# Optimization experiments

Measured on AMD Instinct MI355X. Metric: run time of the kernel, lower is better.

The kernel has to match this reference:

```python
import jax, jax.numpy as jnp
import numpy as np

N = 50000   # nodes
E = 800000  # edges
D = 256     # num_features == embedding_num
L = 3       # gcn layers
G = 512     # graphs in batch


def setup_inputs() -> dict:
    key = jax.random.key(0)
    ks = jax.random.split(key, 7)
    x = jax.random.normal(ks[0], (N, D), dtype=jnp.float32)
    edge_index = jax.random.randint(ks[1], (2, E), 0, N, dtype=jnp.int32)
    batch = jnp.sort(jax.random.randint(ks[2], (N,), 0, G, dtype=jnp.int32))
    s = 0.05
    Ws1 = jax.random.normal(ks[3], (L, D, D), dtype=jnp.float32) * s
    bs1 = jnp.zeros((L, D), dtype=jnp.float32)
    Ws2 = jax.random.normal(ks[4], (L, D, D), dtype=jnp.float32) * s
    bs2 = jnp.zeros((L, D), dtype=jnp.float32)
    return {"x": x, "edge_index": edge_index, "batch": batch,
            "Ws1": Ws1, "bs1": bs1, "Ws2": Ws2, "bs2": bs2}


def reference(x, edge_index, batch, Ws1, bs1, Ws2, bs2):
    src, dst = edge_index[0], edge_index[1]
    h = x
    xs = []
    for i in range(L):
        # GINConv (eps=0): h_i' = MLP( h_i + sum_{j->i} h_j )
        agg = h + jax.ops.segment_sum(h[src], dst, num_segments=N)  # [N, D]
        t = jnp.maximum(agg @ Ws1[i] + bs1[i], 0.0)                 # inner ReLU
        h = jnp.maximum(t @ Ws2[i] + bs2[i], 0.0)                   # outer F.relu
        xs.append(h)
    # global mean pool per layer output, keyed by graph id
    ones = jnp.ones((N, 1), dtype=x.dtype)
    counts = jnp.clip(jax.ops.segment_sum(ones, batch, num_segments=G), 1.0)  # [G,1]
    pooled = [jax.ops.segment_sum(h_i, batch, num_segments=G) / counts for h_i in xs]
    graph_embed = jnp.concatenate(pooled, axis=1)  # [G, L*D]
    node_embed = jnp.concatenate(xs, axis=1)       # [N, L*D]
    return graph_embed, node_embed
```

## Files before the change

### kernel.cpp

```cpp
#include <hip/hip_runtime.h>

#define NN 50000
#define EE 800000
#define DD 256
#define LL 3
#define GG 512
#define MPAD 50048

typedef __attribute__((ext_vector_type(4))) _Float16 half4;
typedef __attribute__((ext_vector_type(8))) _Float16 half8;
typedef __attribute__((ext_vector_type(16))) float floatx16;

#define CONV_B 12500
#define WPK_B  192
#define HIST_B 3125

__global__ void k_prep(const float* __restrict__ x, _Float16* __restrict__ h16,
                       const float* __restrict__ Ws1, const float* __restrict__ Ws2,
                       _Float16* __restrict__ Wp,
                       const int* __restrict__ dst, int* __restrict__ deg) {
    int b = blockIdx.x;
    if (b < CONV_B) {
        int i = b * 256 + threadIdx.x;
        if (i >= NN * DD / 4) return;
        float4 v = ((const float4*)x)[i];
        half4 o;
        o.x = (_Float16)v.x; o.y = (_Float16)v.y; o.z = (_Float16)v.z; o.w = (_Float16)v.w;
        ((half4*)h16)[i] = o;
    } else if (b < CONV_B + WPK_B) {
        int tid  = (b - CONV_B) * 256 + threadIdx.x;
        int lane = tid & 63;
        int nb   = (tid >> 6) & 7;
        int ks   = (tid >> 9) & 15;
        int w    = tid >> 13;
        if (w >= 6) return;
        int l = w >> 1, s = w & 1;
        const float* W = (s == 0 ? Ws1 : Ws2) + (size_t)l * DD * DD;
        int kbase = ks * 16 + (lane >> 5) * 8;
        int n     = nb * 32 + (lane & 31);
        half8 hi;
#pragma unroll
        for (int j = 0; j < 8; ++j) hi[j] = (_Float16)W[(size_t)(kbase + j) * DD + n];
        ((half8*)Wp)[(((size_t)w * 16 + ks) * 8 + nb) * 64 + lane] = hi;
    } else {
        int i = (b - CONV_B - WPK_B) * 256 + threadIdx.x;
        if (i < EE) atomicAdd(&deg[dst[i]], 1);
    }
}

__global__ void k_scan1(const int* __restrict__ deg, int* __restrict__ rp,
                        int* __restrict__ bsum, int n) {
    __shared__ int s[1024];
    int t = threadIdx.x;
    int i = blockIdx.x * 1024 + t;
    int v = (i < n) ? deg[i] : 0;
    s[t] = v;
    __syncthreads();
    for (int off = 1; off < 1024; off <<= 1) {
        int tmp = (t >= off) ? s[t - off] : 0;
        __syncthreads();
        s[t] += tmp;
        __syncthreads();
    }
    if (i < n) rp[i] = s[t] - v;
    if (t == 1023) bsum[blockIdx.x] = s[1023];
}

__global__ void k_scan2(int* __restrict__ bsum, int nb, int* __restrict__ total_out) {
    int lane = threadIdx.x & 63;
    int v = (lane < nb) ? bsum[lane] : 0;
    int orig = v;
    for (int off = 1; off < 64; off <<= 1) {
        int u = __shfl_up(v, off);
        if (lane >= off) v += u;
    }
    if (lane < nb) bsum[lane] = v - orig;
    if (lane == 63) *total_out = v;
}

__global__ void k_scan3(int* __restrict__ rp, const int* __restrict__ bsum,
                        int* __restrict__ cursor, int n) {
    int i = blockIdx.x * 1024 + threadIdx.x;
    if (i < n) {
        int v = rp[i] + bsum[blockIdx.x];
        rp[i] = v;
        cursor[i] = v;
    }
}

__global__ void k_scatter(const int* __restrict__ src, const int* __restrict__ dst,
                          int* __restrict__ cursor, int* __restrict__ csr_src, int e) {
    int i = blockIdx.x * blockDim.x + threadIdx.x;
    if (i < e) {
        int d = dst[i];
        int pos = atomicAdd(&cursor[d], 1);
        csr_src[pos] = src[i];
    }
}

__global__ __launch_bounds__(256) void k_gather(
        const _Float16* __restrict__ h,
        const int* __restrict__ row_ptr,
        const int* __restrict__ csr_src,
        _Float16* __restrict__ agg) {
    __shared__ int eidx[1024];
    __shared__ int rp_s[5];
    int t = threadIdx.x, lane = t & 63, w = t >> 6;
    int n0 = blockIdx.x * 4;
    if (t < 5) {
        int nn = n0 + t;
        if (nn > NN) nn = NN;
        rp_s[t] = row_ptr[nn];
    }
    __syncthreads();
    int beg0 = rp_s[0];
    int cnt  = rp_s[4] - beg0;
    for (int i = t; i < cnt && i < 1024; i += 256) eidx[i] = csr_src[beg0 + i];
    __syncthreads();

    int n = n0 + w;
    if (n >= NN) return;
    int beg = rp_s[w] - beg0, end = rp_s[w + 1] - beg0;
    int hf = lane >> 5;
    int cl = lane & 31;
    const half8* hp = (const half8*)h;

    half8 acc;
#pragma unroll
    for (int i = 0; i < 8; ++i) acc[i] = (_Float16)0;
    if (hf == 0) acc = hp[(size_t)n * 32 + cl];

    if (cnt <= 1024) {
        int k = beg;
        for (; k + 16 <= end; k += 16) {
            half8 v[8];
#pragma unroll
            for (int u = 0; u < 8; ++u) {
                int s = eidx[k + 2 * u + hf];
                v[u] = hp[(size_t)s * 32 + cl];
            }
#pragma unroll
            for (int u = 0; u < 8; ++u) acc += v[u];
        }
        if (k < end) {
#pragma unroll
            for (int u = 0; u < 8; ++u) {
                int e = k + 2 * u + hf;
                half8 v;
#pragma unroll
                for (int i = 0; i < 8; ++i) v[i] = (_Float16)0;
                if (e < end) v = hp[(size_t)eidx[e] * 32 + cl];
                acc += v;
            }
        }
    } else {
        int k = beg;
        for (; k + 16 <= end; k += 16) {
            half8 v[8];
#pragma unroll
            for (int u = 0; u < 8; ++u) {
                int s = csr_src[beg0 + k + 2 * u + hf];
                v[u] = hp[(size_t)s * 32 + cl];
            }
#pragma unroll
            for (int u = 0; u < 8; ++u) acc += v[u];
        }
        if (k < end) {
#pragma unroll
            for (int u = 0; u < 8; ++u) {
                int e = k + 2 * u + hf;
                half8 v;
#pragma unroll
                for (int i = 0; i < 8; ++i) v[i] = (_Float16)0;
                if (e < end) v = hp[(size_t)csr_src[beg0 + e] * 32 + cl];
                acc += v;
            }
        }
    }

    int4 ai = *(int4*)&acc;
    int4 bi;
    bi.x = __shfl_xor(ai.x, 32);
    bi.y = __shfl_xor(ai.y, 32);
    bi.z = __shfl_xor(ai.z, 32);
    bi.w = __shfl_xor(ai.w, 32);
    acc += *(half8*)&bi;
    if (hf == 0) ((half8*)(agg + (size_t)n * DD))[cl] = acc;
}

__global__ __launch_bounds__(256) void k_mlp(
        const _Float16* __restrict__ A,
        const int* __restrict__ batch,
        const _Float16* __restrict__ Wp1, const float* __restrict__ b1,
        const _Float16* __restrict__ Wp2, const float* __restrict__ b2,
        _Float16* __restrict__ Hout,
        float* __restrict__ Fout,
        float* __restrict__ Gout) {
    __shared__ _Float16 t_lds[32 * 256];
    __shared__ int batch_s[32];
    int t    = threadIdx.x;
    int lane = t & 63;
    int w    = t >> 6;
    int r0   = blockIdx.x * 32;

    if (t < 32) {
        int r = r0 + t;
        batch_s[t] = (r < NN) ? batch[r] : 0x7fffffff;
    }

    int arow = r0 + (lane & 31);
    const half8* baseA = (const half8*)(A + (size_t)arow * DD) + (lane >> 5);
    const half8* B1    = (const half8*)Wp1;

    floatx16 acc[2];
#pragma unroll
    for (int nt = 0; nt < 2; ++nt)
#pragma unroll
        for (int i = 0; i < 16; ++i) acc[nt][i] = 0.0f;

#pragma unroll 4
    for (int ks = 0; ks < 16; ++ks) {
        half8 a = baseA[ks * 2];
#pragma unroll
        for (int nt = 0; nt < 2; ++nt) {
            half8 b = B1[(size_t)(ks * 8 + w * 2 + nt) * 64 + lane];
            acc[nt] = __builtin_amdgcn_mfma_f32_32x32x16_f16(a, b, acc[nt], 0, 0, 0);
        }
    }

#pragma unroll
    for (int nt = 0; nt < 2; ++nt) {
        int c  = w * 64 + nt * 32 + (lane & 31);
        float bv = b1[c];
#pragma unroll
        for (int reg = 0; reg < 16; ++reg) {
            int lr = (reg & 3) + 8 * (reg >> 2) + 4 * (lane >> 5);
            float v = fmaxf(acc[nt][reg] + bv, 0.0f);
            t_lds[lr * 256 + ((((c >> 3) ^ (lr & 7)) << 3) | (c & 7))] = (_Float16)v;
        }
    }
    __syncthreads();

    const half8* B2 = (const half8*)Wp2;
    int r = lane & 31;
    floatx16 acc2[2];
#pragma unroll
    for (int nt = 0; nt < 2; ++nt)
#pragma unroll
        for (int i = 0; i < 16; ++i) acc2[nt][i] = 0.0f;

#pragma unroll 4
    for (int ks = 0; ks < 16; ++ks) {
        int kblk = ks * 2 + (lane >> 5);
        half8 a = *(const half8*)&t_lds[r * 256 + ((kblk ^ (r & 7)) << 3)];
#pragma unroll
        for (int nt = 0; nt < 2; ++nt) {
            half8 b = B2[(size_t)(ks * 8 + w * 2 + nt) * 64 + lane];
            acc2[nt] = __builtin_amdgcn_mfma_f32_32x32x16_f16(a, b, acc2[nt], 0, 0, 0);
        }
    }

    const int rbase = 4 * (lane >> 5);
#pragma unroll
    for (int nt = 0; nt < 2; ++nt) {
        int col = w * 64 + nt * 32 + (lane & 31);
        float bv = b2[col];
#pragma unroll
        for (int reg = 0; reg < 16; ++reg) {
            int rowid = rbase + (reg & 3) + 8 * (reg >> 2);
            int row = r0 + rowid;
            if (row < NN) {
                float v = fmaxf(acc2[nt][reg] + bv, 0.0f);
                if (Hout) Hout[(size_t)row * DD + col] = (_Float16)v;
                __builtin_nontemporal_store(v, &Fout[(size_t)row * 768 + col]);
            }
        }
    }

    int lastid = NN - 1 - r0;
    if (lastid >= 0) {
        if (lastid > 31) lastid = 31;
        int g0 = batch_s[0];
        int g1 = batch_s[lastid];
        for (int g = g0; g <= g1; ++g) {
#pragma unroll
            for (int nt = 0; nt < 2; ++nt) {
                int col = w * 64 + nt * 32 + (lane & 31);
                float bv = b2[col];
                float s = 0.0f;
#pragma unroll
                for (int reg = 0; reg < 16; ++reg) {
                    int rowid = rbase + (reg & 3) + 8 * (reg >> 2);
                    if (batch_s[rowid] == g)
                        s += fmaxf(acc2[nt][reg] + bv, 0.0f);
                }
                s += __shfl_xor(s, 32);
                if (lane < 32)
                    atomicAdd(&Gout[(size_t)g * 768 + col], s);
            }
        }
    }
}

__global__ void k_pool_final(const float* __restrict__ gsum,
                             const int* __restrict__ batch,
                             float* __restrict__ graph_embed) {
    int g = blockIdx.x;
    int t = threadIdx.x;
    int start, end;
    { int l = 0, h = NN; while (l < h) { int m = (l + h) >> 1; if (batch[m] < g) l = m + 1; else h = m; } start = l; }
    { int l = 0, h = NN; while (l < h) { int m = (l + h) >> 1; if (batch[m] < g + 1) l = m + 1; else h = m; } end = l; }
    int cnt = end - start;
    float inv = 1.0f / (float)(cnt > 0 ? cnt : 1);
    float4 v = ((const float4*)(gsum + (size_t)g * 768))[t];
    float4 o; o.x = v.x * inv; o.y = v.y * inv; o.z = v.z * inv; o.w = v.w * inv;
    ((float4*)(graph_embed + (size_t)g * 768))[t] = o;
}

extern "C" void kernel_launch(void* const* d_in, const int* in_sizes, int n_in,
                              void* d_out, int out_size, void* d_ws, size_t ws_size,
                              hipStream_t stream) {
    const float* x     = (const float*)d_in[0];
    const int*   ei    = (const int*)d_in[1];
    const int*   batch = (const int*)d_in[2];
    const float* Ws1   = (const float*)d_in[3];
    const float* bs1   = (const float*)d_in[4];
    const float* Ws2   = (const float*)d_in[5];
    const float* bs2   = (const float*)d_in[6];

    float* out         = (float*)d_out;
    float* graph_embed = out;
    float* node_embed  = out + (size_t)GG * 768;

    _Float16* h16   = (_Float16*)d_ws;
    _Float16* agg16 = h16 + (size_t)MPAD * DD;
    _Float16* Wp    = agg16 + (size_t)MPAD * DD;
    float* gsum     = (float*)(Wp + (size_t)6 * 65536);
    int* cursor     = (int*)(gsum + (size_t)GG * 768);
    int* bsum       = cursor + NN;
    int* csr_src    = bsum + 64;
    int* row_ptr    = csr_src + EE;

    const int* src = ei;
    const int* dst = ei + EE;

    const int NB = (NN + 1023) / 1024;

    hipMemsetAsync(gsum, 0, (size_t)GG * 768 * 4 + (size_t)NN * 4 + 64 * 4, stream);

    k_prep<<<CONV_B + WPK_B + HIST_B, 256, 0, stream>>>(x, h16, Ws1, Ws2, Wp, dst, cursor);

    k_scan1<<<NB, 1024, 0, stream>>>(cursor, row_ptr, bsum, NN);
    k_scan2<<<1, 64, 0, stream>>>(bsum, NB, row_ptr + NN);
    k_scan3<<<NB, 1024, 0, stream>>>(row_ptr, bsum, cursor, NN);
    k_scatter<<<(EE + 255) / 256, 256, 0, stream>>>(src, dst, cursor, csr_src, EE);

    for (int l = 0; l < LL; ++l) {
        k_gather<<<(NN + 3) / 4, 256, 0, stream>>>(h16, row_ptr, csr_src, agg16);
        k_mlp<<<MPAD / 32, 256, 0, stream>>>(
            agg16, batch,
            Wp + (size_t)(2 * l + 0) * 65536, bs1 + (size_t)l * DD,
            Wp + (size_t)(2 * l + 1) * 65536, bs2 + (size_t)l * DD,
            (l == LL - 1) ? nullptr : h16,
            node_embed + (size_t)l * DD, gsum + (size_t)l * DD);
    }

    k_pool_final<<<GG, 192, 0, stream>>>(gsum, batch, graph_embed);
}
```

Measured before the change: 594.8 us.

## Pipeline gather and MLP across node chunks in a combined kernel

Splits each layer's node range into four chunks and launches a combined kernel whose blocks either run the MLP on the previous chunk or gather the next chunk. The goal is to overlap the memory-bound gather with the compute-bound MLP instead of running them as separate full-size launches. The hidden state is now double-buffered (h16/h_alt) so the next layer's output is not written while another chunk still reads the current layer's input. This adds launches per layer and uses more shared memory per block in the combined kernel, which may lower occupancy.

```diff
diff --git a/kernel.cpp b/kernel.cpp
--- a/kernel.cpp
+++ b/kernel.cpp
@@ -6,6 +6,9 @@
 #define LL 3
 #define GG 512
 #define MPAD 50048
+#define RPC  12512
+#define GB   (RPC / 4)
+#define MB   (RPC / 32)
 
 typedef __attribute__((ext_vector_type(4))) _Float16 half4;
 typedef __attribute__((ext_vector_type(8))) _Float16 half8;
@@ -98,15 +101,12 @@
     }
 }
 
-__global__ __launch_bounds__(256) void k_gather(
+__device__ __forceinline__ void gather_body(
         const _Float16* __restrict__ h,
         const int* __restrict__ row_ptr,
         const int* __restrict__ csr_src,
-        _Float16* __restrict__ agg) {
-    __shared__ int eidx[1024];
-    __shared__ int rp_s[5];
+        _Float16* agg, int n0, int* eidx, int* rp_s) {
     int t = threadIdx.x, lane = t & 63, w = t >> 6;
-    int n0 = blockIdx.x * 4;
     if (t < 5) {
         int nn = n0 + t;
         if (nn > NN) nn = NN;
@@ -188,20 +188,16 @@
     if (hf == 0) ((half8*)(agg + (size_t)n * DD))[cl] = acc;
 }
 
-__global__ __launch_bounds__(256) void k_mlp(
+__device__ __forceinline__ void mlp_body(
         const _Float16* __restrict__ A,
         const int* __restrict__ batch,
         const _Float16* __restrict__ Wp1, const float* __restrict__ b1,
         const _Float16* __restrict__ Wp2, const float* __restrict__ b2,
-        _Float16* __restrict__ Hout,
-        float* __restrict__ Fout,
-        float* __restrict__ Gout) {
-    __shared__ _Float16 t_lds[32 * 256];
-    __shared__ int batch_s[32];
+        _Float16* Hout, float* __restrict__ Fout, float* __restrict__ Gout,
+        int r0, _Float16* t_lds, int* batch_s) {
     int t    = threadIdx.x;
     int lane = t & 63;
     int w    = t >> 6;
-    int r0   = blockIdx.x * 32;
 
     if (t < 32) {
         int r = r0 + t;
@@ -299,6 +295,47 @@
                     atomicAdd(&Gout[(size_t)g * 768 + col], s);
             }
         }
+    }
+}
+
+__global__ __launch_bounds__(256) void k_gather(
+        const _Float16* __restrict__ h, const int* __restrict__ row_ptr,
+        const int* __restrict__ csr_src, _Float16* agg, int nbeg) {
+    __shared__ int eidx[1024];
+    __shared__ int rp_s[5];
+    gather_body(h, row_ptr, csr_src, agg, nbeg + blockIdx.x * 4, eidx, rp_s);
+}
+
+__global__ __launch_bounds__(256) void k_mlp(
+        const _Float16* __restrict__ A, const int* __restrict__ batch,
+        const _Float16* __restrict__ Wp1, const float* __restrict__ b1,
+        const _Float16* __restrict__ Wp2, const float* __restrict__ b2,
+        _Float16* Hout, float* __restrict__ Fout, float* __restrict__ Gout,
+        int rbeg) {
+    __shared__ _Float16 t_lds[32 * 256];
+    __shared__ int batch_s[32];
+    mlp_body(A, batch, Wp1, b1, Wp2, b2, Hout, Fout, Gout,
+             rbeg + blockIdx.x * 32, t_lds, batch_s);
+}
+
+__global__ __launch_bounds__(256) void k_gm(
+        const _Float16* __restrict__ hin, const int* __restrict__ row_ptr,
+        const int* __restrict__ csr_src, _Float16* agg,
+        const int* __restrict__ batch,
+        const _Float16* __restrict__ Wp1, const float* __restrict__ b1,
+        const _Float16* __restrict__ Wp2, const float* __restrict__ b2,
+        _Float16* Hout, float* __restrict__ Fout, float* __restrict__ Gout,
+        int mlp_blocks, int mlp_rbeg, int gather_nbeg) {
+    __shared__ _Float16 t_lds[32 * 256];
+    __shared__ int batch_s[32];
+    __shared__ int eidx[1024];
+    __shared__ int rp_s[5];
+    if ((int)blockIdx.x < mlp_blocks) {
+        mlp_body(agg, batch, Wp1, b1, Wp2, b2, Hout, Fout, Gout,
+                 mlp_rbeg + blockIdx.x * 32, t_lds, batch_s);
+    } else {
+        gather_body(hin, row_ptr, csr_src, agg,
+                    gather_nbeg + (blockIdx.x - mlp_blocks) * 4, eidx, rp_s);
     }
 }
 
@@ -333,7 +370,8 @@
     float* node_embed  = out + (size_t)GG * 768;
 
     _Float16* h16   = (_Float16*)d_ws;
-    _Float16* agg16 = h16 + (size_t)MPAD * DD;
+    _Float16* h_alt = h16 + (size_t)MPAD * DD;
+    _Float16* agg16 = h_alt + (size_t)MPAD * DD;
     _Float16* Wp    = agg16 + (size_t)MPAD * DD;
     float* gsum     = (float*)(Wp + (size_t)6 * 65536);
     int* cursor     = (int*)(gsum + (size_t)GG * 768);
@@ -356,13 +394,23 @@
     k_scatter<<<(EE + 255) / 256, 256, 0, stream>>>(src, dst, cursor, csr_src, EE);
 
     for (int l = 0; l < LL; ++l) {
-        k_gather<<<(NN + 3) / 4, 256, 0, stream>>>(h16, row_ptr, csr_src, agg16);
-        k_mlp<<<MPAD / 32, 256, 0, stream>>>(
-            agg16, batch,
-            Wp + (size_t)(2 * l + 0) * 65536, bs1 + (size_t)l * DD,
-            Wp + (size_t)(2 * l + 1) * 65536, bs2 + (size_t)l * DD,
-            (l == LL - 1) ? nullptr : h16,
-            node_embed + (size_t)l * DD, gsum + (size_t)l * DD);
+        const _Float16* hin  = (l & 1) ? h_alt : h16;
+        _Float16*       hout = (l == LL - 1) ? nullptr : ((l & 1) ? h16 : h_alt);
+        const _Float16* W1 = Wp + (size_t)(2 * l + 0) * 65536;
+        const _Float16* W2 = Wp + (size_t)(2 * l + 1) * 65536;
+        const float* bb1 = bs1 + (size_t)l * DD;
+        const float* bb2 = bs2 + (size_t)l * DD;
+        float* F  = node_embed + (size_t)l * DD;
+        float* Gp = gsum + (size_t)l * DD;
+
+        k_gather<<<GB, 256, 0, stream>>>(hin, row_ptr, csr_src, agg16, 0);
+        for (int c = 0; c < 3; ++c)
+            k_gm<<<MB + GB, 256, 0, stream>>>(
+                hin, row_ptr, csr_src, agg16, batch,
+                W1, bb1, W2, bb2, hout, F, Gp,
+                MB, c * RPC, (c + 1) * RPC);
+        k_mlp<<<MB, 256, 0, stream>>>(agg16, batch, W1, bb1, W2, bb2,
+                                      hout, F, Gp, 3 * RPC);
     }
 
     k_pool_final<<<GG, 192, 0, stream>>>(gsum, batch, graph_embed);
```

New measurement: 607.7 us. +2.2%, slower.

## Fuse neighbor gather into MLP kernel with ping-pong feature buffers

Applied to the files above, without the earlier changes.

The separate gather and MLP kernels are merged into one per-layer kernel. Each 32-row block now aggregates its own node neighborhoods straight into LDS and feeds that tile to the first MFMA GEMM. This removes the agg16 round trip through global memory and one launch per layer. Because blocks now read h while others write it, the layer input and output alternate between two buffers. In exchange, each block has only 4 waves serially gathering 8 nodes each, which may reduce memory-level parallelism compared with the former 12500-block gather.

```diff
diff --git a/kernel.cpp b/kernel.cpp
--- a/kernel.cpp
+++ b/kernel.cpp
@@ -6,6 +6,7 @@
 #define LL 3
 #define GG 512
 #define MPAD 50048
+#define FB   1563
 
 typedef __attribute__((ext_vector_type(4))) _Float16 half4;
 typedef __attribute__((ext_vector_type(8))) _Float16 half8;
@@ -98,98 +99,10 @@
     }
 }
 
-__global__ __launch_bounds__(256) void k_gather(
-        const _Float16* __restrict__ h,
+__global__ __launch_bounds__(256) void k_layer(
+        const _Float16* __restrict__ hin,
         const int* __restrict__ row_ptr,
         const int* __restrict__ csr_src,
-        _Float16* __restrict__ agg) {
-    __shared__ int eidx[1024];
-    __shared__ int rp_s[5];
-    int t = threadIdx.x, lane = t & 63, w = t >> 6;
-    int n0 = blockIdx.x * 4;
-    if (t < 5) {
-        int nn = n0 + t;
-        if (nn > NN) nn = NN;
-        rp_s[t] = row_ptr[nn];
-    }
-    __syncthreads();
-    int beg0 = rp_s[0];
-    int cnt  = rp_s[4] - beg0;
-    for (int i = t; i < cnt && i < 1024; i += 256) eidx[i] = csr_src[beg0 + i];
-    __syncthreads();
-
-    int n = n0 + w;
-    if (n >= NN) return;
-    int beg = rp_s[w] - beg0, end = rp_s[w + 1] - beg0;
-    int hf = lane >> 5;
-    int cl = lane & 31;
-    const half8* hp = (const half8*)h;
-
-    half8 acc;
-#pragma unroll
-    for (int i = 0; i < 8; ++i) acc[i] = (_Float16)0;
-    if (hf == 0) acc = hp[(size_t)n * 32 + cl];
-
-    if (cnt <= 1024) {
-        int k = beg;
-        for (; k + 16 <= end; k += 16) {
-            half8 v[8];
-#pragma unroll
-            for (int u = 0; u < 8; ++u) {
-                int s = eidx[k + 2 * u + hf];
-                v[u] = hp[(size_t)s * 32 + cl];
-            }
-#pragma unroll
-            for (int u = 0; u < 8; ++u) acc += v[u];
-        }
-        if (k < end) {
-#pragma unroll
-            for (int u = 0; u < 8; ++u) {
-                int e = k + 2 * u + hf;
-                half8 v;
-#pragma unroll
-                for (int i = 0; i < 8; ++i) v[i] = (_Float16)0;
-                if (e < end) v = hp[(size_t)eidx[e] * 32 + cl];
-                acc += v;
-            }
-        }
-    } else {
-        int k = beg;
-        for (; k + 16 <= end; k += 16) {
-            half8 v[8];
-#pragma unroll
-            for (int u = 0; u < 8; ++u) {
-                int s = csr_src[beg0 + k + 2 * u + hf];
-                v[u] = hp[(size_t)s * 32 + cl];
-            }
-#pragma unroll
-            for (int u = 0; u < 8; ++u) acc += v[u];
-        }
-        if (k < end) {
-#pragma unroll
-            for (int u = 0; u < 8; ++u) {
-                int e = k + 2 * u + hf;
-                half8 v;
-#pragma unroll
-                for (int i = 0; i < 8; ++i) v[i] = (_Float16)0;
-                if (e < end) v = hp[(size_t)csr_src[beg0 + e] * 32 + cl];
-                acc += v;
-            }
-        }
-    }
-
-    int4 ai = *(int4*)&acc;
-    int4 bi;
-    bi.x = __shfl_xor(ai.x, 32);
-    bi.y = __shfl_xor(ai.y, 32);
-    bi.z = __shfl_xor(ai.z, 32);
-    bi.w = __shfl_xor(ai.w, 32);
-    acc += *(half8*)&bi;
-    if (hf == 0) ((half8*)(agg + (size_t)n * DD))[cl] = acc;
-}
-
-__global__ __launch_bounds__(256) void k_mlp(
-        const _Float16* __restrict__ A,
         const int* __restrict__ batch,
         const _Float16* __restrict__ Wp1, const float* __restrict__ b1,
         const _Float16* __restrict__ Wp2, const float* __restrict__ b2,
@@ -197,36 +110,123 @@
         float* __restrict__ Fout,
         float* __restrict__ Gout) {
     __shared__ _Float16 t_lds[32 * 256];
+    __shared__ int eidx[1536];
+    __shared__ int rp_s[33];
     __shared__ int batch_s[32];
     int t    = threadIdx.x;
     int lane = t & 63;
     int w    = t >> 6;
     int r0   = blockIdx.x * 32;
 
-    if (t < 32) {
-        int r = r0 + t;
-        batch_s[t] = (r < NN) ? batch[r] : 0x7fffffff;
-    }
-
-    int arow = r0 + (lane & 31);
-    const half8* baseA = (const half8*)(A + (size_t)arow * DD) + (lane >> 5);
-    const half8* B1    = (const half8*)Wp1;
-
-    floatx16 acc[2];
+    if (t < 33) {
+        int nn = r0 + t;
+        if (nn > NN) nn = NN;
+        rp_s[t] = row_ptr[nn];
+    }
+    if (t >= 64 && t < 96) {
+        int r = r0 + (t - 64);
+        batch_s[t - 64] = (r < NN) ? batch[r] : 0x7fffffff;
+    }
+    __syncthreads();
+    int beg0 = rp_s[0];
+    int cnt  = rp_s[32] - beg0;
+    for (int i = t; i < cnt && i < 1536; i += 256) eidx[i] = csr_src[beg0 + i];
+    __syncthreads();
+
+    int hf = lane >> 5;
+    int cl = lane & 31;
+    const half8* hp = (const half8*)hin;
+    for (int i = 0; i < 8; ++i) {
+        int lr = w * 8 + i;
+        int n  = r0 + lr;
+        if (n >= NN) break;
+        int beg = rp_s[lr] - beg0, end = rp_s[lr + 1] - beg0;
+
+        half8 acc;
+#pragma unroll
+        for (int q = 0; q < 8; ++q) acc[q] = (_Float16)0;
+        if (hf == 0) acc = hp[(size_t)n * 32 + cl];
+
+        if (end <= 1536) {
+            int k = beg;
+            for (; k + 16 <= end; k += 16) {
+                half8 v[8];
+#pragma unroll
+                for (int u = 0; u < 8; ++u) {
+                    int s = eidx[k + 2 * u + hf];
+                    v[u] = hp[(size_t)s * 32 + cl];
+                }
+#pragma unroll
+                for (int u = 0; u < 8; ++u) acc += v[u];
+            }
+            if (k < end) {
+#pragma unroll
+                for (int u = 0; u < 8; ++u) {
+                    int e = k + 2 * u + hf;
+                    half8 v;
+#pragma unroll
+                    for (int q = 0; q < 8; ++q) v[q] = (_Float16)0;
+                    if (e < end) v = hp[(size_t)eidx[e] * 32 + cl];
+                    acc += v;
+                }
+            }
+        } else {
+            int k = beg;
+            for (; k + 16 <= end; k += 16) {
+                half8 v[8];
+#pragma unroll
+                for (int u = 0; u < 8; ++u) {
+                    int s = csr_src[beg0 + k + 2 * u + hf];
+                    v[u] = hp[(size_t)s * 32 + cl];
+                }
+#pragma unroll
+                for (int u = 0; u < 8; ++u) acc += v[u];
+            }
+            if (k < end) {
+#pragma unroll
+                for (int u = 0; u < 8; ++u) {
+                    int e = k + 2 * u + hf;
+                    half8 v;
+#pragma unroll
+                    for (int q = 0; q < 8; ++q) v[q] = (_Float16)0;
+                    if (e < end) v = hp[(size_t)csr_src[beg0 + e] * 32 + cl];
+                    acc += v;
+                }
+            }
+        }
+
+        int4 ai = *(int4*)&acc;
+        int4 bi;
+        bi.x = __shfl_xor(ai.x, 32);
+        bi.y = __shfl_xor(ai.y, 32);
+        bi.z = __shfl_xor(ai.z, 32);
+        bi.w = __shfl_xor(ai.w, 32);
+        acc += *(half8*)&bi;
+        if (hf == 0)
+            *(half8*)&t_lds[lr * 256 + ((cl ^ (lr & 7)) << 3)] = acc;
+    }
+    __syncthreads();
+
+    const half8* B1 = (const half8*)Wp1;
+    int rr = lane & 31;
+
+    floatx16 acc1[2];
 #pragma unroll
     for (int nt = 0; nt < 2; ++nt)
 #pragma unroll
-        for (int i = 0; i < 16; ++i) acc[nt][i] = 0.0f;
+        for (int i = 0; i < 16; ++i) acc1[nt][i] = 0.0f;
 
 #pragma unroll 4
     for (int ks = 0; ks < 16; ++ks) {
-        half8 a = baseA[ks * 2];
+        int kblk = ks * 2 + (lane >> 5);
+        half8 a = *(const half8*)&t_lds[rr * 256 + ((kblk ^ (rr & 7)) << 3)];
 #pragma unroll
         for (int nt = 0; nt < 2; ++nt) {
             half8 b = B1[(size_t)(ks * 8 + w * 2 + nt) * 64 + lane];
-            acc[nt] = __builtin_amdgcn_mfma_f32_32x32x16_f16(a, b, acc[nt], 0, 0, 0);
-        }
-    }
+            acc1[nt] = __builtin_amdgcn_mfma_f32_32x32x16_f16(a, b, acc1[nt], 0, 0, 0);
+        }
+    }
+    __syncthreads();
 
 #pragma unroll
     for (int nt = 0; nt < 2; ++nt) {
@@ -235,14 +235,13 @@
 #pragma unroll
         for (int reg = 0; reg < 16; ++reg) {
             int lr = (reg & 3) + 8 * (reg >> 2) + 4 * (lane >> 5);
-            float v = fmaxf(acc[nt][reg] + bv, 0.0f);
+            float v = fmaxf(acc1[nt][reg] + bv, 0.0f);
             t_lds[lr * 256 + ((((c >> 3) ^ (lr & 7)) << 3) | (c & 7))] = (_Float16)v;
         }
     }
     __syncthreads();
 
     const half8* B2 = (const half8*)Wp2;
-    int r = lane & 31;
     floatx16 acc2[2];
 #pragma unroll
     for (int nt = 0; nt < 2; ++nt)
@@ -252,7 +251,7 @@
 #pragma unroll 4
     for (int ks = 0; ks < 16; ++ks) {
         int kblk = ks * 2 + (lane >> 5);
-        half8 a = *(const half8*)&t_lds[r * 256 + ((kblk ^ (r & 7)) << 3)];
+        half8 a = *(const half8*)&t_lds[rr * 256 + ((kblk ^ (rr & 7)) << 3)];
 #pragma unroll
         for (int nt = 0; nt < 2; ++nt) {
             half8 b = B2[(size_t)(ks * 8 + w * 2 + nt) * 64 + lane];
@@ -333,8 +332,8 @@
     float* node_embed  = out + (size_t)GG * 768;
 
     _Float16* h16   = (_Float16*)d_ws;
-    _Float16* agg16 = h16 + (size_t)MPAD * DD;
-    _Float16* Wp    = agg16 + (size_t)MPAD * DD;
+    _Float16* h_alt = h16 + (size_t)MPAD * DD;
+    _Float16* Wp    = h_alt + (size_t)MPAD * DD;
     float* gsum     = (float*)(Wp + (size_t)6 * 65536);
     int* cursor     = (int*)(gsum + (size_t)GG * 768);
     int* bsum       = cursor + NN;
@@ -356,13 +355,13 @@
     k_scatter<<<(EE + 255) / 256, 256, 0, stream>>>(src, dst, cursor, csr_src, EE);
 
     for (int l = 0; l < LL; ++l) {
-        k_gather<<<(NN + 3) / 4, 256, 0, stream>>>(h16, row_ptr, csr_src, agg16);
-        k_mlp<<<MPAD / 32, 256, 0, stream>>>(
-            agg16, batch,
+        const _Float16* hin  = (l & 1) ? h_alt : h16;
+        _Float16*       hout = (l == LL - 1) ? nullptr : ((l & 1) ? h16 : h_alt);
+        k_layer<<<FB, 256, 0, stream>>>(
+            hin, row_ptr, csr_src, batch,
             Wp + (size_t)(2 * l + 0) * 65536, bs1 + (size_t)l * DD,
             Wp + (size_t)(2 * l + 1) * 65536, bs2 + (size_t)l * DD,
-            (l == LL - 1) ? nullptr : h16,
-            node_embed + (size_t)l * DD, gsum + (size_t)l * DD);
+            hout, node_embed + (size_t)l * DD, gsum + (size_t)l * DD);
     }
 
     k_pool_final<<<GG, 192, 0, stream>>>(gsum, batch, graph_embed);
```

Result: faster. 529.6 us (-11.0%).
